# Kernel optimization log

Measured on AMD Instinct MI355X. Metric: run time of the kernel, lower is better.

Reference implementation:

```python
import jax, jax.numpy as jnp
import numpy as np

D_MODEL, N_GROUPS, N_EXPERTS = 512, 8, 8
TOP_K_L1, TOP_K_L2 = 2, 2
BATCH, SEQ = 2, 512


def setup_inputs() -> dict:
    key = jax.random.key(0)
    ks = jax.random.split(key, 6)
    d, G, E = D_MODEL, N_GROUPS, N_EXPERTS
    scale = 0.02
    x = jax.random.normal(ks[0], (BATCH, SEQ, d), dtype=jnp.float32)
    g1 = jax.random.normal(ks[1], (d, G), dtype=jnp.float32) * scale          # level-1 gate (no bias)
    g2 = jax.random.normal(ks[2], (G, d, E), dtype=jnp.float32) * scale       # per-group level-2 gate (no bias)
    W1 = jax.random.normal(ks[3], (G, E, d, 2 * d), dtype=jnp.float32) * scale
    b1 = jnp.zeros((G, E, 2 * d), dtype=jnp.float32)
    W2 = jax.random.normal(ks[4], (G, E, 2 * d, d), dtype=jnp.float32) * scale
    b2 = jnp.zeros((G, E, d), dtype=jnp.float32)
    return {"x": x, "g1": g1, "g2": g2, "W1": W1, "b1": b1, "W2": W2, "b2": b2}


def reference(x, g1, g2, W1, b1, W2, b2):
    B, S, d = x.shape
    G, E = g1.shape[1], g2.shape[2]
    xt = x.reshape(-1, d)  # [T, d]

    # ---- level-1 routing (groups) ----
    logits1 = xt @ g1                                   # [T, G]
    v1, i1 = jax.lax.top_k(logits1, TOP_K_L1)           # [T, k1]
    w1 = jax.nn.softmax(v1.astype(jnp.float32), axis=-1).astype(x.dtype)
    # dense combine weights: top-k indices are unique per token, so one-hot sum
    # is exactly the original gather/index_add_ math.
    c1 = jnp.sum(jax.nn.one_hot(i1, G, dtype=x.dtype) * w1[..., None], axis=1)  # [T, G]

    # ---- level-2 routing (experts within each group) ----
    logits2 = jnp.einsum('td,gde->tge', xt, g2)         # [T, G, E]
    v2, i2 = jax.lax.top_k(logits2, TOP_K_L2)           # [T, G, k2]
    w2 = jax.nn.softmax(v2.astype(jnp.float32), axis=-1).astype(x.dtype)
    c2 = jnp.sum(jax.nn.one_hot(i2, E, dtype=x.dtype) * w2[..., None], axis=2)  # [T, G, E]

    # ---- expert MLPs (Linear -> ReLU -> Linear), all experts, combined by weights ----
    h = jax.nn.relu(jnp.einsum('td,gedh->tgeh', xt, W1) + b1)   # [T, G, E, 2d]
    y = jnp.einsum('tgeh,gehd->tged', h, W2) + b2               # [T, G, E, d]

    group_out = jnp.einsum('tged,tge->tgd', y, c2)              # level-2 combine
    out = jnp.einsum('tgd,tg->td', group_out, c1)               # level-1 combine
    return out.reshape(B, S, d)
```

## Files before the change

### kernel.cpp

```cpp
#include <hip/hip_runtime.h>
#include <hip/hip_bf16.h>

#define D_M   512
#define H_M   1024
#define G_N   8
#define E_N   8
#define T_N   1024
#define NEXP  64
#define CAP   1024

#define LDK   520

typedef __attribute__((ext_vector_type(8))) short bf16x8;
typedef __attribute__((ext_vector_type(4))) float f32x4;
typedef __attribute__((ext_vector_type(4))) unsigned int u32x4;

__device__ __forceinline__ unsigned pack2(float a, float b) {
  unsigned r;
  asm("v_cvt_pk_bf16_f32 %0, %1, %2" : "=v"(r) : "v"(a), "v"(b));
  return r;
}
__device__ __forceinline__ unsigned short f2bf(float f) {
  unsigned u = __builtin_bit_cast(unsigned, f);
  u = (u + 0x7fffu + ((u >> 16) & 1u)) >> 16;
  return (unsigned short)u;
}

__global__ __launch_bounds__(64) void k_route(
    const float* __restrict__ x, const float* __restrict__ g1,
    const float* __restrict__ g2, float* __restrict__ slotW,
    int* __restrict__ counts, int* __restrict__ list) {
  __shared__ float xs[D_M];
  __shared__ float l2s[G_N][E_N];
  __shared__ float l1s[G_N];
  __shared__ float l1part[G_N][8];
  const int t = blockIdx.x;
  const int lane = threadIdx.x;
  const float* xr = x + (size_t)t * D_M;
  for (int i = lane; i < D_M; i += 64) xs[i] = xr[i];
  __syncthreads();
  {
    const int g = lane >> 3, e = lane & 7;
    const float* gp = g2 + (size_t)g * D_M * E_N + e;
    float acc = 0.f;
    #pragma unroll 8
    for (int i = 0; i < D_M; i++) acc += xs[i] * gp[(size_t)i * E_N];
    l2s[g][e] = acc;
  }
  {
    const int g = lane >> 3, c = lane & 7;
    float acc = 0.f;
    #pragma unroll 8
    for (int i = c * 64; i < c * 64 + 64; i++) acc += xs[i] * g1[(size_t)i * G_N + g];
    l1part[g][c] = acc;
  }
  __syncthreads();
  if (lane < G_N) {
    float s = 0.f;
    #pragma unroll
    for (int c = 0; c < 8; c++) s += l1part[lane][c];
    l1s[lane] = s;
  }
  __syncthreads();
  if (lane == 0) {
    int a1 = 0;
    for (int g = 1; g < G_N; g++) if (l1s[g] > l1s[a1]) a1 = g;
    int a2 = (a1 == 0) ? 1 : 0;
    for (int g = 0; g < G_N; g++) if (g != a1 && l1s[g] > l1s[a2]) a2 = g;
    const float m = l1s[a1];
    float w1a = __expf(l1s[a1] - m), w1b = __expf(l1s[a2] - m);
    const float inv = 1.f / (w1a + w1b);
    w1a *= inv; w1b *= inv;
    const int gsel[2] = {a1, a2};
    const float wsel[2] = {w1a, w1b};
    for (int a = 0; a < 2; a++) {
      const int g = gsel[a];
      int e1 = 0;
      for (int e = 1; e < E_N; e++) if (l2s[g][e] > l2s[g][e1]) e1 = e;
      int e2 = (e1 == 0) ? 1 : 0;
      for (int e = 0; e < E_N; e++) if (e != e1 && l2s[g][e] > l2s[g][e2]) e2 = e;
      const float mm = l2s[g][e1];
      float ua = __expf(l2s[g][e1] - mm), ub = __expf(l2s[g][e2] - mm);
      const float uin = 1.f / (ua + ub);
      ua *= uin; ub *= uin;
      const int ge0 = g * E_N + e1;
      const int ge1 = g * E_N + e2;
      slotW[t * 4 + a * 2 + 0] = wsel[a] * ua;
      slotW[t * 4 + a * 2 + 1] = wsel[a] * ub;
      int p0 = atomicAdd(&counts[ge0], 1);
      list[ge0 * CAP + p0] = t * 4 + a * 2 + 0;
      int p1 = atomicAdd(&counts[ge1], 1);
      list[ge1 * CAP + p1] = t * 4 + a * 2 + 1;
    }
  }
}

__global__ __launch_bounds__(256, 1) void k_mlp1(
    const float* __restrict__ x, const float* __restrict__ W1,
    const float* __restrict__ b1, const int* __restrict__ counts,
    const int* __restrict__ list, unsigned short* __restrict__ h_ws) {
  const int ge = blockIdx.x >> 3;
  const int jt = blockIdx.x & 7;
  const int j0 = jt * 128;
  const int n = counts[ge];
  if (n == 0) return;
  __shared__ unsigned short xl[64 * LDK];
  __shared__ int tokTS[64];
  const int tid = threadIdx.x;
  const int lane = tid & 63, wave = tid >> 6;
  const int m16 = lane & 15, quad = lane >> 4;

  const float* Wcol = W1 + (size_t)ge * (D_M * H_M) + j0 + wave * 32 + m16;
  float bv[2];
  #pragma unroll
  for (int nt = 0; nt < 2; nt++) bv[nt] = b1[ge * H_M + j0 + wave * 32 + nt * 16 + m16];

  bf16x8 wf0[16], wf1[16];
  #pragma unroll
  for (int s = 0; s < 16; s++) {
    float v[8], w[8];
    #pragma unroll
    for (int i = 0; i < 8; i++) v[i] = Wcol[(size_t)(s * 32 + quad * 8 + i) * H_M];
    #pragma unroll
    for (int i = 0; i < 8; i++) w[i] = Wcol[(size_t)(s * 32 + quad * 8 + i) * H_M + 16];
    u32x4 pa = { pack2(v[0], v[1]), pack2(v[2], v[3]), pack2(v[4], v[5]), pack2(v[6], v[7]) };
    u32x4 pb = { pack2(w[0], w[1]), pack2(w[2], w[3]), pack2(w[4], w[5]), pack2(w[6], w[7]) };
    wf0[s] = __builtin_bit_cast(bf16x8, pa);
    wf1[s] = __builtin_bit_cast(bf16x8, pb);
  }

  for (int t0 = 0; t0 < n; t0 += 64) {
    __syncthreads();
    if (tid < 64) {
      int idx = t0 + tid;
      tokTS[tid] = list[ge * CAP + (idx < n ? idx : n - 1)];
    }
    __syncthreads();
    {
      const int trow = tid >> 2;
      const int kb = (tid & 3) * 4;
      const float* xr = x + (size_t)(tokTS[trow] >> 2) * D_M + kb;
      unsigned short* dst = &xl[trow * LDK + kb];
      #pragma unroll 8
      for (int rep = 0; rep < 32; rep++) {
        f32x4 v = *(const f32x4*)(xr + rep * 16);
        uint2 p = { pack2(v.x, v.y), pack2(v.z, v.w) };
        *(uint2*)(dst + rep * 16) = p;
      }
    }
    __syncthreads();

    f32x4 acc[4][2] = {};
    #pragma unroll
    for (int s = 0; s < 16; s++) {
      #pragma unroll
      for (int mt = 0; mt < 4; mt++) {
        bf16x8 af = *(bf16x8*)&xl[(mt * 16 + m16) * LDK + s * 32 + quad * 8];
        acc[mt][0] = __builtin_amdgcn_mfma_f32_16x16x32_bf16(af, wf0[s], acc[mt][0], 0, 0, 0);
        acc[mt][1] = __builtin_amdgcn_mfma_f32_16x16x32_bf16(af, wf1[s], acc[mt][1], 0, 0, 0);
      }
    }
    #pragma unroll
    for (int mt = 0; mt < 4; mt++)
      #pragma unroll
      for (int i = 0; i < 4; i++) {
        const int tr = mt * 16 + quad * 4 + i;
        if (t0 + tr < n) {
          const int ts = tokTS[tr];
          unsigned short* hp = h_ws + (size_t)ts * H_M + j0 + wave * 32 + m16;
          #pragma unroll
          for (int nt = 0; nt < 2; nt++) {
            float v = acc[mt][nt][i] + bv[nt];
            hp[nt * 16] = f2bf(v > 0.f ? v : 0.f);
          }
        }
      }
  }
}

__global__ __launch_bounds__(256, 1) void k_mlp2(
    const unsigned short* __restrict__ h_ws, const float* __restrict__ W2,
    const float* __restrict__ b2, const int* __restrict__ counts,
    const int* __restrict__ list, float* __restrict__ y0,
    float* __restrict__ y1) {
  const int ge = blockIdx.x >> 3;
  const int jtile = (blockIdx.x >> 1) & 3;
  const int j0 = jtile * 128;
  const int ks = blockIdx.x & 1;
  const int n = counts[ge];
  if (n == 0) return;
  __shared__ unsigned short xl[64 * LDK];
  __shared__ int tokTS[64];
  const int tid = threadIdx.x;
  const int lane = tid & 63, wave = tid >> 6;
  const int m16 = lane & 15, quad = lane >> 4;

  const float* Wcol = W2 + (size_t)ge * (H_M * D_M) + (size_t)(ks * 512) * D_M + j0 + wave * 32 + m16;
  float bv[2];
  #pragma unroll
  for (int nt = 0; nt < 2; nt++)
    bv[nt] = ks == 0 ? b2[ge * D_M + j0 + wave * 32 + nt * 16 + m16] : 0.f;
  float* yk = ks == 0 ? y0 : y1;

  bf16x8 wf0[16], wf1[16];
  #pragma unroll
  for (int s = 0; s < 16; s++) {
    float v[8], w[8];
    #pragma unroll
    for (int i = 0; i < 8; i++) v[i] = Wcol[(size_t)(s * 32 + quad * 8 + i) * D_M];
    #pragma unroll
    for (int i = 0; i < 8; i++) w[i] = Wcol[(size_t)(s * 32 + quad * 8 + i) * D_M + 16];
    u32x4 pa = { pack2(v[0], v[1]), pack2(v[2], v[3]), pack2(v[4], v[5]), pack2(v[6], v[7]) };
    u32x4 pb = { pack2(w[0], w[1]), pack2(w[2], w[3]), pack2(w[4], w[5]), pack2(w[6], w[7]) };
    wf0[s] = __builtin_bit_cast(bf16x8, pa);
    wf1[s] = __builtin_bit_cast(bf16x8, pb);
  }

  for (int t0 = 0; t0 < n; t0 += 64) {
    __syncthreads();
    if (tid < 64) {
      int idx = t0 + tid;
      tokTS[tid] = list[ge * CAP + (idx < n ? idx : n - 1)];
    }
    __syncthreads();
    {
      const int trow = tid >> 2;
      const int kb = (tid & 3) * 8;
      const unsigned short* hr = h_ws + (size_t)tokTS[trow] * H_M + ks * 512 + kb;
      unsigned short* dst = &xl[trow * LDK + kb];
      #pragma unroll 8
      for (int rep = 0; rep < 16; rep++)
        *(u32x4*)(dst + rep * 32) = *(const u32x4*)(hr + rep * 32);
    }
    __syncthreads();

    f32x4 acc[4][2] = {};
    #pragma unroll
    for (int s = 0; s < 16; s++) {
      #pragma unroll
      for (int mt = 0; mt < 4; mt++) {
        bf16x8 af = *(bf16x8*)&xl[(mt * 16 + m16) * LDK + s * 32 + quad * 8];
        acc[mt][0] = __builtin_amdgcn_mfma_f32_16x16x32_bf16(af, wf0[s], acc[mt][0], 0, 0, 0);
        acc[mt][1] = __builtin_amdgcn_mfma_f32_16x16x32_bf16(af, wf1[s], acc[mt][1], 0, 0, 0);
      }
    }
    #pragma unroll
    for (int mt = 0; mt < 4; mt++)
      #pragma unroll
      for (int i = 0; i < 4; i++) {
        const int tr = mt * 16 + quad * 4 + i;
        if (t0 + tr < n) {
          const int ts = tokTS[tr];
          float* yp = yk + (size_t)ts * D_M + j0 + wave * 32 + m16;
          #pragma unroll
          for (int nt = 0; nt < 2; nt++)
            yp[nt * 16] = acc[mt][nt][i] + bv[nt];
        }
      }
  }
}

__global__ __launch_bounds__(256) void k_combine(
    const float* __restrict__ y0, const float* __restrict__ y1,
    const float* __restrict__ slotW, float* __restrict__ out) {
  const int idx = blockIdx.x * 256 + threadIdx.x;
  if (idx >= T_N * D_M / 4) return;
  const int t = idx >> 7;
  const int j = (idx & 127) * 4;
  float4 r = {0.f, 0.f, 0.f, 0.f};
  #pragma unroll
  for (int s = 0; s < 4; s++) {
    const float w = slotW[t * 4 + s];
    const size_t off = (size_t)(t * 4 + s) * D_M + j;
    const float4 a = *(const float4*)(y0 + off);
    const float4 b = *(const float4*)(y1 + off);
    r.x += w * (a.x + b.x);
    r.y += w * (a.y + b.y);
    r.z += w * (a.z + b.z);
    r.w += w * (a.w + b.w);
  }
  *(float4*)&out[(size_t)t * D_M + j] = r;
}

extern "C" void kernel_launch(void* const* d_in, const int* in_sizes, int n_in,
                              void* d_out, int out_size, void* d_ws, size_t ws_size,
                              hipStream_t stream) {
  const float* x  = (const float*)d_in[0];
  const float* g1 = (const float*)d_in[1];
  const float* g2 = (const float*)d_in[2];
  const float* W1 = (const float*)d_in[3];
  const float* b1 = (const float*)d_in[4];
  const float* W2 = (const float*)d_in[5];
  const float* b2 = (const float*)d_in[6];
  float* out = (float*)d_out;

  char* ws = (char*)d_ws;
  float*          slotW  = (float*)(ws + 16384);
  int*            counts = (int*)(ws + 32768);
  int*            list   = (int*)(ws + 36864);
  unsigned short* h_ws   = (unsigned short*)(ws + 524288);
  float*          y0     = (float*)(ws + 524288 + 8388608);
  float*          y1     = (float*)(ws + 524288 + 16777216);

  hipMemsetAsync(counts, 0, NEXP * sizeof(int), stream);
  k_route<<<T_N, 64, 0, stream>>>(x, g1, g2, slotW, counts, list);
  k_mlp1<<<NEXP * 8, 256, 0, stream>>>(x, W1, b1, counts, list, h_ws);
  k_mlp2<<<NEXP * 8, 256, 0, stream>>>(h_ws, W2, b2, counts, list, y0, y1);
  k_combine<<<(T_N * D_M / 4) / 256, 256, 0, stream>>>(y0, y1, slotW, out);
}
```

Before: 375.0 us.

## Stage expert weights through LDS with coalesced loads and halve per-block column tile

The two MLP kernels used to load expert weights with strided scalar global reads straight into register fragments. They now read them as coalesced float4 rows, convert to bf16 and scatter into an LDS buffer in MFMA fragment order, which each wave then reads per k-step. The column tile per block drops from 128 to 64, so the grid doubles to 1024 blocks for more parallelism and fewer live registers. The cost is more LDS use per block, scattered 2-byte LDS writes with possible bank conflicts, and each token tile being staged twice as often across blocks.

New measurement: 390.8 us. 4.2% more time.

```diff
diff --git a/kernel.cpp b/kernel.cpp
--- a/kernel.cpp
+++ b/kernel.cpp
@@ -99,34 +99,38 @@
     const float* __restrict__ x, const float* __restrict__ W1,
     const float* __restrict__ b1, const int* __restrict__ counts,
     const int* __restrict__ list, unsigned short* __restrict__ h_ws) {
-  const int ge = blockIdx.x >> 3;
-  const int jt = blockIdx.x & 7;
-  const int j0 = jt * 128;
+  const int ge = blockIdx.x >> 4;
+  const int jt = blockIdx.x & 15;
+  const int jbase = jt * 64;
   const int n = counts[ge];
   if (n == 0) return;
+  __shared__ unsigned short wl[4 * 16 * 64 * 8];
   __shared__ unsigned short xl[64 * LDK];
   __shared__ int tokTS[64];
   const int tid = threadIdx.x;
   const int lane = tid & 63, wave = tid >> 6;
   const int m16 = lane & 15, quad = lane >> 4;
 
-  const float* Wcol = W1 + (size_t)ge * (D_M * H_M) + j0 + wave * 32 + m16;
-  float bv[2];
-  #pragma unroll
-  for (int nt = 0; nt < 2; nt++) bv[nt] = b1[ge * H_M + j0 + wave * 32 + nt * 16 + m16];
-
-  bf16x8 wf0[16], wf1[16];
-  #pragma unroll
-  for (int s = 0; s < 16; s++) {
-    float v[8], w[8];
-    #pragma unroll
-    for (int i = 0; i < 8; i++) v[i] = Wcol[(size_t)(s * 32 + quad * 8 + i) * H_M];
-    #pragma unroll
-    for (int i = 0; i < 8; i++) w[i] = Wcol[(size_t)(s * 32 + quad * 8 + i) * H_M + 16];
-    u32x4 pa = { pack2(v[0], v[1]), pack2(v[2], v[3]), pack2(v[4], v[5]), pack2(v[6], v[7]) };
-    u32x4 pb = { pack2(w[0], w[1]), pack2(w[2], w[3]), pack2(w[4], w[5]), pack2(w[6], w[7]) };
-    wf0[s] = __builtin_bit_cast(bf16x8, pa);
-    wf1[s] = __builtin_bit_cast(bf16x8, pb);
+  const float bv = b1[ge * H_M + jbase + wave * 16 + m16];
+
+  {
+    const float* Wg = W1 + (size_t)ge * (D_M * H_M) + jbase;
+    const int rgrp = tid >> 4;
+    const int lidx = tid & 15;
+    const int wp = lidx >> 2;
+    const int m16b = (lidx & 3) * 4;
+    #pragma unroll 4
+    for (int pass = 0; pass < 32; pass++) {
+      const int r = pass * 16 + rgrp;
+      f32x4 v = *(const f32x4*)(Wg + (size_t)r * H_M + lidx * 4);
+      const int s = r >> 5, q = (r >> 3) & 3, i = r & 7;
+      unsigned p0 = pack2(v.x, v.y), p1 = pack2(v.z, v.w);
+      unsigned short* base = &wl[((wp * 16 + s) * 64 + q * 16 + m16b) * 8 + i];
+      base[0 * 8] = (unsigned short)p0;
+      base[1 * 8] = (unsigned short)(p0 >> 16);
+      base[2 * 8] = (unsigned short)p1;
+      base[3 * 8] = (unsigned short)(p1 >> 16);
+    }
   }
 
   for (int t0 = 0; t0 < n; t0 += 64) {
@@ -150,14 +154,14 @@
     }
     __syncthreads();
 
-    f32x4 acc[4][2] = {};
+    f32x4 acc[4] = {};
     #pragma unroll
     for (int s = 0; s < 16; s++) {
+      bf16x8 wfrag = *(const bf16x8*)&wl[((wave * 16 + s) * 64 + lane) * 8];
       #pragma unroll
       for (int mt = 0; mt < 4; mt++) {
         bf16x8 af = *(bf16x8*)&xl[(mt * 16 + m16) * LDK + s * 32 + quad * 8];
-        acc[mt][0] = __builtin_amdgcn_mfma_f32_16x16x32_bf16(af, wf0[s], acc[mt][0], 0, 0, 0);
-        acc[mt][1] = __builtin_amdgcn_mfma_f32_16x16x32_bf16(af, wf1[s], acc[mt][1], 0, 0, 0);
+        acc[mt] = __builtin_amdgcn_mfma_f32_16x16x32_bf16(af, wfrag, acc[mt], 0, 0, 0);
       }
     }
     #pragma unroll
@@ -167,12 +171,8 @@
         const int tr = mt * 16 + quad * 4 + i;
         if (t0 + tr < n) {
           const int ts = tokTS[tr];
-          unsigned short* hp = h_ws + (size_t)ts * H_M + j0 + wave * 32 + m16;
-          #pragma unroll
-          for (int nt = 0; nt < 2; nt++) {
-            float v = acc[mt][nt][i] + bv[nt];
-            hp[nt * 16] = f2bf(v > 0.f ? v : 0.f);
-          }
+          float v = acc[mt][i] + bv;
+          h_ws[(size_t)ts * H_M + jbase + wave * 16 + m16] = f2bf(v > 0.f ? v : 0.f);
         }
       }
   }
@@ -183,37 +183,40 @@
     const float* __restrict__ b2, const int* __restrict__ counts,
     const int* __restrict__ list, float* __restrict__ y0,
     float* __restrict__ y1) {
-  const int ge = blockIdx.x >> 3;
-  const int jtile = (blockIdx.x >> 1) & 3;
-  const int j0 = jtile * 128;
+  const int ge = blockIdx.x >> 4;
+  const int jt = (blockIdx.x >> 1) & 7;
+  const int jbase = jt * 64;
   const int ks = blockIdx.x & 1;
   const int n = counts[ge];
   if (n == 0) return;
+  __shared__ unsigned short wl[4 * 16 * 64 * 8];
   __shared__ unsigned short xl[64 * LDK];
   __shared__ int tokTS[64];
   const int tid = threadIdx.x;
   const int lane = tid & 63, wave = tid >> 6;
   const int m16 = lane & 15, quad = lane >> 4;
 
-  const float* Wcol = W2 + (size_t)ge * (H_M * D_M) + (size_t)(ks * 512) * D_M + j0 + wave * 32 + m16;
-  float bv[2];
-  #pragma unroll
-  for (int nt = 0; nt < 2; nt++)
-    bv[nt] = ks == 0 ? b2[ge * D_M + j0 + wave * 32 + nt * 16 + m16] : 0.f;
+  const float bv = ks == 0 ? b2[ge * D_M + jbase + wave * 16 + m16] : 0.f;
   float* yk = ks == 0 ? y0 : y1;
 
-  bf16x8 wf0[16], wf1[16];
-  #pragma unroll
-  for (int s = 0; s < 16; s++) {
-    float v[8], w[8];
-    #pragma unroll
-    for (int i = 0; i < 8; i++) v[i] = Wcol[(size_t)(s * 32 + quad * 8 + i) * D_M];
-    #pragma unroll
-    for (int i = 0; i < 8; i++) w[i] = Wcol[(size_t)(s * 32 + quad * 8 + i) * D_M + 16];
-    u32x4 pa = { pack2(v[0], v[1]), pack2(v[2], v[3]), pack2(v[4], v[5]), pack2(v[6], v[7]) };
-    u32x4 pb = { pack2(w[0], w[1]), pack2(w[2], w[3]), pack2(w[4], w[5]), pack2(w[6], w[7]) };
-    wf0[s] = __builtin_bit_cast(bf16x8, pa);
-    wf1[s] = __builtin_bit_cast(bf16x8, pb);
+  {
+    const float* Wg = W2 + (size_t)ge * (H_M * D_M) + (size_t)(ks * 512) * D_M + jbase;
+    const int rgrp = tid >> 4;
+    const int lidx = tid & 15;
+    const int wp = lidx >> 2;
+    const int m16b = (lidx & 3) * 4;
+    #pragma unroll 4
+    for (int pass = 0; pass < 32; pass++) {
+      const int r = pass * 16 + rgrp;
+      f32x4 v = *(const f32x4*)(Wg + (size_t)r * D_M + lidx * 4);
+      const int s = r >> 5, q = (r >> 3) & 3, i = r & 7;
+      unsigned p0 = pack2(v.x, v.y), p1 = pack2(v.z, v.w);
+      unsigned short* base = &wl[((wp * 16 + s) * 64 + q * 16 + m16b) * 8 + i];
+      base[0 * 8] = (unsigned short)p0;
+      base[1 * 8] = (unsigned short)(p0 >> 16);
+      base[2 * 8] = (unsigned short)p1;
+      base[3 * 8] = (unsigned short)(p1 >> 16);
+    }
   }
 
   for (int t0 = 0; t0 < n; t0 += 64) {
@@ -234,14 +237,14 @@
     }
     __syncthreads();
 
-    f32x4 acc[4][2] = {};
+    f32x4 acc[4] = {};
     #pragma unroll
     for (int s = 0; s < 16; s++) {
+      bf16x8 wfrag = *(const bf16x8*)&wl[((wave * 16 + s) * 64 + lane) * 8];
       #pragma unroll
       for (int mt = 0; mt < 4; mt++) {
         bf16x8 af = *(bf16x8*)&xl[(mt * 16 + m16) * LDK + s * 32 + quad * 8];
-        acc[mt][0] = __builtin_amdgcn_mfma_f32_16x16x32_bf16(af, wf0[s], acc[mt][0], 0, 0, 0);
-        acc[mt][1] = __builtin_amdgcn_mfma_f32_16x16x32_bf16(af, wf1[s], acc[mt][1], 0, 0, 0);
+        acc[mt] = __builtin_amdgcn_mfma_f32_16x16x32_bf16(af, wfrag, acc[mt], 0, 0, 0);
       }
     }
     #pragma unroll
@@ -251,10 +254,7 @@
         const int tr = mt * 16 + quad * 4 + i;
         if (t0 + tr < n) {
           const int ts = tokTS[tr];
-          float* yp = yk + (size_t)ts * D_M + j0 + wave * 32 + m16;
-          #pragma unroll
-          for (int nt = 0; nt < 2; nt++)
-            yp[nt * 16] = acc[mt][nt][i] + bv[nt];
+          yk[(size_t)ts * D_M + jbase + wave * 16 + m16] = acc[mt][i] + bv;
         }
       }
   }
@@ -304,7 +304,7 @@
 
   hipMemsetAsync(counts, 0, NEXP * sizeof(int), stream);
   k_route<<<T_N, 64, 0, stream>>>(x, g1, g2, slotW, counts, list);
-  k_mlp1<<<NEXP * 8, 256, 0, stream>>>(x, W1, b1, counts, list, h_ws);
-  k_mlp2<<<NEXP * 8, 256, 0, stream>>>(h_ws, W2, b2, counts, list, y0, y1);
+  k_mlp1<<<NEXP * 16, 256, 0, stream>>>(x, W1, b1, counts, list, h_ws);
+  k_mlp2<<<NEXP * 16, 256, 0, stream>>>(h_ws, W2, b2, counts, list, y0, y1);
   k_combine<<<(T_N * D_M / 4) / 256, 256, 0, stream>>>(y0, y1, slotW, out);
 }
```
